# Kernel optimization log

Measured on AMD Instinct MI355X. Metric: run time of the kernel, lower is better.

Reference implementation:

```python
import jax, jax.numpy as jnp
import numpy as np

MASK_FILL = -1e9  # masked_fill_value (avoids NaNs vs -inf)

def setup_inputs() -> dict:
    key = jax.random.key(0)
    k1, k2, k3 = jax.random.split(key, 3)
    B, L, H, E = 4, 2048, 16, 128
    S, D = L, E
    queries = jax.random.normal(k1, (B, L, H, E), dtype=jnp.float32)
    keys = jax.random.normal(k2, (B, S, H, E), dtype=jnp.float32)
    values = jax.random.normal(k3, (B, S, H, D), dtype=jnp.float32)
    return {"queries": queries, "keys": keys, "values": values}

def reference(queries, keys, values):
    B, L, H, E = queries.shape
    S = keys.shape[1]
    scale = 1.0 / jnp.sqrt(jnp.asarray(E, queries.dtype))
    # compute_scores: dot-product scores (B,H,L,S)
    scores = jnp.einsum('blhe,bshe->bhls', queries, keys)
    # causal mask (mask_flag=True, attn_mask=None -> TriangularCausalMask)
    causal = jnp.triu(jnp.ones((L, S), dtype=bool), k=1)  # True above diagonal = masked
    scores = jnp.where(causal[None, None, :, :], MASK_FILL, scores)
    # scale * scores -> softmax (dropout p=0, eval)
    A = jax.nn.softmax(scale * scores, axis=-1)
    # combine_values: (B,H,L,S) x (B,S,H,D) -> (B,L,H,D)
    V = jnp.einsum('bhls,bshd->blhd', A, values)
    return V
```

## Files before the change

### kernel.cpp

```cpp
#include <hip/hip_runtime.h>
#include <hip/hip_bf16.h>

typedef __attribute__((ext_vector_type(4))) float f32x4;
typedef __attribute__((ext_vector_type(2))) float f32x2v;
typedef __attribute__((ext_vector_type(16))) float f32x16;
typedef __attribute__((ext_vector_type(8))) short s16x8;
typedef __attribute__((ext_vector_type(4))) short s16x4;
typedef __attribute__((ext_vector_type(4))) unsigned u32x4v;
typedef __attribute__((ext_vector_type(2))) int i32x2;

static constexpr int Bb = 4, Ll = 2048, Hh = 16, Ee = 128;
static constexpr int RS = Hh * Ee;
static constexpr float SCALE = 0.088388347648318447f;
static constexpr float LOG2E = 1.4426950408889634f;
static constexpr float SCL = SCALE * LOG2E;
static constexpr float MOFF = 26.0f;

static constexpr int KROW = 272;
static constexpr int KBYTES = 32 * KROW;
static constexpr int VROW = 80;
static constexpr int VBYTES = 128 * VROW;
static constexpr int BUFSZ = KBYTES + VBYTES;

__device__ __forceinline__ unsigned pk2bf(float lo, float hi) {
  float2 t = make_float2(lo, hi);
  __hip_bfloat162 b2 = __float22bfloat162_rn(t);
  union { __hip_bfloat162 b; unsigned u; } cv; cv.b = b2;
  return cv.u;
}

__device__ __forceinline__ s16x8 pack8(float a0, float a1, float a2, float a3,
                                       float a4, float a5, float a6, float a7) {
  u32x4v u = { pk2bf(a0,a1), pk2bf(a2,a3), pk2bf(a4,a5), pk2bf(a6,a7) };
  return *(s16x8*)&u;
}

__device__ __forceinline__ void plswap(int &x, int &y, int h5) {
#if __has_builtin(__builtin_amdgcn_permlane32_swap)
  i32x2 r = __builtin_amdgcn_permlane32_swap(x, y, false, false);
  x = r[0]; y = r[1];
#else
  int px = __shfl_xor(x, 32, 64);
  int py = __shfl_xor(y, 32, 64);
  int nx = h5 ? py : x;
  int ny = h5 ? y : px;
  x = nx; y = ny;
#endif
}

__device__ __forceinline__ s16x8 mkpa(float p0, float p1, float p2, float p3,
                                      float p4, float p5, float p6, float p7, int h5) {
  int uA = (int)pk2bf(p0, p1), uB = (int)pk2bf(p2, p3);
  int uC = (int)pk2bf(p4, p5), uD = (int)pk2bf(p6, p7);
  plswap(uA, uC, h5);
  plswap(uB, uD, h5);
  u32x4v u = { (unsigned)uA, (unsigned)uB, (unsigned)uC, (unsigned)uD };
  return *(s16x8*)&u;
}

__device__ __forceinline__ void gl_lds16(const short* g, short* l) {
  __builtin_amdgcn_global_load_lds((const __attribute__((address_space(1))) void*)g,
                                   (__attribute__((address_space(3))) void*)l, 16, 0, 0);
}

__global__ __launch_bounds__(256) void conv_k(const float* __restrict__ src, short* __restrict__ dst) {
  size_t i = ((size_t)blockIdx.x * 256 + threadIdx.x) * 8;
  f32x4 a = *(const f32x4*)(src + i);
  f32x4 b = *(const f32x4*)(src + i + 4);
  *(s16x8*)(dst + i) = pack8(a[0],a[1],a[2],a[3],b[0],b[1],b[2],b[3]);
}

__global__ __launch_bounds__(256) void conv_vt(const float* __restrict__ V, unsigned* __restrict__ Vt32) {
  const int bh = blockIdx.x >> 4, s0 = (blockIdx.x & 15) * 128;
  const int b = bh >> 4, h = bh & 15;
  const int w = threadIdx.x >> 6, lane = threadIdx.x & 63;
  const float* base = V + ((size_t)(b * Ll + s0 + 32 * w)) * RS + h * Ee + 2 * lane;
  unsigned w0[16], w1[16];
#pragma unroll
  for (int j = 0; j < 16; ++j) {
    f32x2v a = *(const f32x2v*)(base + (size_t)(2 * j) * RS);
    f32x2v c = *(const f32x2v*)(base + (size_t)(2 * j + 1) * RS);
    w0[j] = pk2bf(a[0], c[0]);
    w1[j] = pk2bf(a[1], c[1]);
  }
  unsigned* r0 = Vt32 + ((size_t)(bh * 128 + 2 * lane)) * 1024 + (s0 + 32 * w) / 2;
  unsigned* r1 = r0 + 1024;
#pragma unroll
  for (int jj = 0; jj < 4; ++jj) {
    *(u32x4v*)(r0 + 4 * jj) = (u32x4v){w0[4*jj], w0[4*jj+1], w0[4*jj+2], w0[4*jj+3]};
    *(u32x4v*)(r1 + 4 * jj) = (u32x4v){w1[4*jj], w1[4*jj+1], w1[4*jj+2], w1[4*jj+3]};
  }
}

__global__ __launch_bounds__(256, 3)
void attn_main(const float* __restrict__ Qg, const short* __restrict__ Kws,
               const short* __restrict__ Vtws, float* __restrict__ Og) {
  const int phys = blockIdx.x;
  const int qi = ((phys >> 6) & 1) ? (phys >> 7) : (15 - (phys >> 7));
  const int bh = phys & 63;
  const int b = bh >> 4, h = bh & 15;
  const int qb = qi * 128;
  const int tid = threadIdx.x, w = tid >> 6, l = tid & 63;
  const int l31 = l & 31, h5 = l >> 5;

  __shared__ __align__(16) short smem[BUFSZ];

  s16x8 qfrag[8];
  {
    const float* qp = Qg + ((size_t)(b * Ll + qb + 32 * w + l31)) * RS + h * Ee;
#pragma unroll
    for (int ks = 0; ks < 8; ++ks) {
      const int e0 = 16 * ks + 8 * h5;
      f32x4 f0 = *(const f32x4*)(qp + e0);
      f32x4 f1 = *(const f32x4*)(qp + e0 + 4);
      qfrag[ks] = pack8(f0[0]*SCL, f0[1]*SCL, f0[2]*SCL, f0[3]*SCL,
                        f1[0]*SCL, f1[1]*SCL, f1[2]*SCL, f1[3]*SCL);
    }
  }

  f32x16 acc[4];
#pragma unroll
  for (int dt = 0; dt < 4; ++dt)
#pragma unroll
    for (int r = 0; r < 16; ++r) acc[dt][r] = 0.f;
  float lacc = 0.f;

  const short* skp[3]; const short* svp[3];
  int kdst[3], vdst[3];
#pragma unroll
  for (int j = 0; j < 3; ++j) {
    const int kid = (j < 2) ? (w * 136 + 64 * j + l) : (w * 136 + 128 + (l & 7));
    const int kr = kid / 17;
    int ksl = kid % 17; if (ksl == 16) ksl = 0;
    skp[j] = Kws + ((size_t)(b * Ll + kr)) * 2048 + h * 128 + ksl * 8;
    kdst[j] = kid * 16;
    const int vid = (j < 2) ? (w * 160 + 64 * j + l) : (w * 160 + 128 + (l & 31));
    const int vr = vid / 5;
    int vsl = vid % 5; if (vsl == 4) vsl = 0;
    svp[j] = Vtws + ((size_t)(bh * 128 + vr)) * 2048 + vsl * 8;
    vdst[j] = KBYTES + vid * 16;
  }

#define STAGE(cb, kvb) do { \
    gl_lds16(skp[0] + (size_t)(kvb) * 2048, (short*)((char*)smem + (cb) + kdst[0])); \
    gl_lds16(skp[1] + (size_t)(kvb) * 2048, (short*)((char*)smem + (cb) + kdst[1])); \
    if (l < 8)  gl_lds16(skp[2] + (size_t)(kvb) * 2048, (short*)((char*)smem + (cb) + kdst[2])); \
    gl_lds16(svp[0] + (kvb), (short*)((char*)smem + (cb) + vdst[0])); \
    gl_lds16(svp[1] + (kvb), (short*)((char*)smem + (cb) + vdst[1])); \
    if (l < 32) gl_lds16(svp[2] + (kvb), (short*)((char*)smem + (cb) + vdst[2])); \
  } while (0)

  const int ntiles = 4 * qi + 4;
  const int tmaxw = 4 * qi + w;

  STAGE(0, 0);

  for (int t = 0; t < ntiles; ++t) {
    const int cbase = (t & 1) ? BUFSZ : 0;
    if (t + 1 < ntiles) {
      STAGE(cbase ? 0 : BUFSZ, 32 * (t + 1));
      asm volatile("s_waitcnt vmcnt(6)" ::: "memory");
    } else {
      asm volatile("s_waitcnt vmcnt(0)" ::: "memory");
    }
    __builtin_amdgcn_s_barrier();
    __builtin_amdgcn_sched_barrier(0);

    if (t <= tmaxw) {
      f32x16 s;
#pragma unroll
      for (int r = 0; r < 16; ++r) s[r] = 0.f;
      __builtin_amdgcn_s_setprio(1);
#pragma unroll
      for (int ks = 0; ks < 8; ++ks) {
        s16x8 a = *(const s16x8*)((const char*)smem + cbase + l31 * KROW + h5 * 16 + ks * 32);
        s = __builtin_amdgcn_mfma_f32_32x32x16_bf16(a, qfrag[ks], s, 0, 0, 0);
      }
      __builtin_amdgcn_s_setprio(0);

      if (t == tmaxw) {
#pragma unroll
        for (int r = 0; r < 16; ++r) {
          const int kvl = (r & 3) + 8 * (r >> 2) + 4 * h5;
          if (kvl > l31) s[r] = -3.0e38f;
        }
      }

      float pv[16];
#pragma unroll
      for (int r = 0; r < 16; ++r) { const float p2 = exp2f(s[r] - MOFF); pv[r] = p2; lacc += p2; }
      s16x8 pa0 = mkpa(pv[0], pv[1], pv[2], pv[3], pv[4], pv[5], pv[6], pv[7], h5);
      s16x8 pa1 = mkpa(pv[8], pv[9], pv[10], pv[11], pv[12], pv[13], pv[14], pv[15], h5);

      __builtin_amdgcn_s_setprio(1);
#pragma unroll
      for (int dt = 0; dt < 4; ++dt) {
        const int vb = cbase + KBYTES + dt * (32 * VROW) + l31 * VROW + h5 * 16;
        s16x8 av0 = *(const s16x8*)((const char*)smem + vb);
        acc[dt] = __builtin_amdgcn_mfma_f32_32x32x16_bf16(av0, pa0, acc[dt], 0, 0, 0);
        s16x8 av1 = *(const s16x8*)((const char*)smem + vb + 32);
        acc[dt] = __builtin_amdgcn_mfma_f32_32x32x16_bf16(av1, pa1, acc[dt], 0, 0, 0);
      }
      __builtin_amdgcn_s_setprio(0);
    }
    __builtin_amdgcn_sched_barrier(0);
    __builtin_amdgcn_s_barrier();
  }
#undef STAGE

  float lsum;
  {
    int pb = __builtin_bit_cast(int, lacc), pc = pb;
    plswap(pb, pc, h5);
    lsum = __builtin_bit_cast(float, pb) + __builtin_bit_cast(float, pc);
  }
  const float linv = 1.0f / lsum;

  float* orow = Og + ((size_t)(b * Ll + qb + 32 * w + l31)) * RS + h * Ee;
#pragma unroll
  for (int dt = 0; dt < 4; ++dt)
#pragma unroll
    for (int g = 0; g < 4; ++g) {
      f32x4 v = { acc[dt][4*g] * linv, acc[dt][4*g+1] * linv,
                  acc[dt][4*g+2] * linv, acc[dt][4*g+3] * linv };
      *(f32x4*)(orow + dt * 32 + g * 8 + h5 * 4) = v;
    }
}

static constexpr int VPAD = 66;
__device__ __forceinline__ short f2bf(float f) {
  union { float f; unsigned u; } x; x.f = f;
  unsigned r = x.u + 0x7FFFu + ((x.u >> 16) & 1u);
  return (short)(r >> 16);
}
__global__ __launch_bounds__(256, 4)
void attn_fwd(const float* __restrict__ Qg, const float* __restrict__ Kg,
              const float* __restrict__ Vg, float* __restrict__ Og) {
  const int qi = blockIdx.x;
  const int bh = blockIdx.y;
  const int b = bh >> 4, h = bh & 15;
  const int qb = qi * 64;
  const int tid = threadIdx.x, wave = tid >> 6, lane = tid & 63, lo = lane & 15, hi = lane >> 4;
  __shared__ __align__(16) short Klds[64 * 128];
  __shared__ __align__(16) short Vt[128 * VPAD];
  const float* Qb_ = Qg + (size_t)b * Ll * RS + h * Ee;
  const float* Kb_ = Kg + (size_t)b * Ll * RS + h * Ee;
  const float* Vb_ = Vg + (size_t)b * Ll * RS + h * Ee;
  float* Ob_ = Og + (size_t)b * Ll * RS + h * Ee;
  s16x8 qfrag[4];
  {
    const float* qp = Qb_ + (size_t)(qb + wave * 16 + lo) * RS;
#pragma unroll
    for (int ks = 0; ks < 4; ++ks) {
      const int e0 = 32 * ks + 8 * hi;
      f32x4 f0 = *(const f32x4*)(qp + e0);
      f32x4 f1 = *(const f32x4*)(qp + e0 + 4);
      qfrag[ks] = pack8(f0[0]*SCALE, f0[1]*SCALE, f0[2]*SCALE, f0[3]*SCALE,
                        f1[0]*SCALE, f1[1]*SCALE, f1[2]*SCALE, f1[3]*SCALE);
    }
  }
  f32x4 acc[8];
#pragma unroll
  for (int nt = 0; nt < 8; ++nt) acc[nt] = (f32x4){0.f, 0.f, 0.f, 0.f};
  float mrun = -3.0e38f, lrun = 0.f;
  const int r0 = tid >> 4, c0 = (tid & 15) * 8;
  for (int kvb = 0; kvb <= qb; kvb += 64) {
    __syncthreads();
#pragma unroll
    for (int rr4 = 0; rr4 < 4; ++rr4) {
      const int rr = r0 + 16 * rr4;
      const float* kp = Kb_ + (size_t)(kvb + rr) * RS + c0;
      f32x4 f0 = *(const f32x4*)kp;
      f32x4 f1 = *(const f32x4*)(kp + 4);
      const int off = (rr * 256 + c0 * 2) ^ ((rr & 7) << 4);
      *(s16x8*)((char*)Klds + off) = pack8(f0[0],f0[1],f0[2],f0[3],f1[0],f1[1],f1[2],f1[3]);
    }
#pragma unroll
    for (int kk = 0; kk < 2; ++kk) {
      const int kv0 = (r0 * 2 + kk) * 2;
      const float* vp0 = Vb_ + (size_t)(kvb + kv0) * RS + c0;
      const float* vp1 = vp0 + RS;
      f32x4 a0 = *(const f32x4*)vp0, a1 = *(const f32x4*)(vp0 + 4);
      f32x4 b0 = *(const f32x4*)vp1, b1 = *(const f32x4*)(vp1 + 4);
#pragma unroll
      for (int j = 0; j < 4; ++j)
        *(unsigned*)&Vt[(c0 + j) * VPAD + kv0] = pk2bf(a0[j], b0[j]);
#pragma unroll
      for (int j = 0; j < 4; ++j)
        *(unsigned*)&Vt[(c0 + 4 + j) * VPAD + kv0] = pk2bf(a1[j], b1[j]);
    }
    __syncthreads();
    const bool diag = (kvb == qb);
    f32x4 st[4];
#pragma unroll
    for (int mt = 0; mt < 4; ++mt) {
      f32x4 a4 = (f32x4){0.f, 0.f, 0.f, 0.f};
#pragma unroll
      for (int ks = 0; ks < 4; ++ks) {
        const int row = 16 * mt + lo;
        const int off = (row * 256 + (32 * ks + 8 * hi) * 2) ^ ((row & 7) << 4);
        s16x8 a = *(const s16x8*)((const char*)Klds + off);
        a4 = __builtin_amdgcn_mfma_f32_16x16x32_bf16(a, qfrag[ks], a4, 0, 0, 0);
      }
      st[mt] = a4;
    }
    if (diag) {
      const int qg = 16 * wave + lo;
#pragma unroll
      for (int mt = 0; mt < 4; ++mt)
#pragma unroll
        for (int r = 0; r < 4; ++r)
          if (16 * mt + 4 * hi + r > qg) st[mt][r] = -3.0e38f;
    }
    float mx = -3.0e38f;
#pragma unroll
    for (int mt = 0; mt < 4; ++mt)
#pragma unroll
      for (int r = 0; r < 4; ++r) mx = fmaxf(mx, st[mt][r]);
    mx = fmaxf(mx, __shfl_xor(mx, 16, 64));
    mx = fmaxf(mx, __shfl_xor(mx, 32, 64));
    const float mnew = fmaxf(mrun, mx);
    const float alpha = exp2f((mrun - mnew) * LOG2E);
    float psum = 0.f;
    s16x4 pf[4];
#pragma unroll
    for (int mt = 0; mt < 4; ++mt)
#pragma unroll
      for (int r = 0; r < 4; ++r) {
        const float p = exp2f((st[mt][r] - mnew) * LOG2E);
        psum += p;
        pf[mt][r] = f2bf(p);
      }
    psum += __shfl_xor(psum, 16, 64);
    psum += __shfl_xor(psum, 32, 64);
    lrun = lrun * alpha + psum;
    mrun = mnew;
    float alr[4];
#pragma unroll
    for (int r = 0; r < 4; ++r) alr[r] = __shfl(alpha, 4 * hi + r, 64);
#pragma unroll
    for (int nt = 0; nt < 8; ++nt) {
      acc[nt][0] *= alr[0]; acc[nt][1] *= alr[1];
      acc[nt][2] *= alr[2]; acc[nt][3] *= alr[3];
    }
#pragma unroll
    for (int mt = 0; mt < 4; ++mt)
#pragma unroll
      for (int nt = 0; nt < 8; ++nt) {
        const int hw = (16 * nt + lo) * VPAD + 16 * mt + 4 * hi;
        s16x4 vf = *(const s16x4*)&Vt[hw];
        acc[nt] = __builtin_amdgcn_mfma_f32_16x16x16bf16_1k(pf[mt], vf, acc[nt], 0, 0, 0);
      }
  }
  float linv[4];
#pragma unroll
  for (int r = 0; r < 4; ++r) linv[r] = 1.0f / __shfl(lrun, 4 * hi + r, 64);
#pragma unroll
  for (int r = 0; r < 4; ++r) {
    const int qg = qb + 16 * wave + 4 * hi + r;
    float* op = Ob_ + (size_t)qg * RS + lo;
#pragma unroll
    for (int nt = 0; nt < 8; ++nt)
      op[16 * nt] = acc[nt][r] * linv[r];
  }
}

extern "C" void kernel_launch(void* const* d_in, const int* in_sizes, int n_in,
                              void* d_out, int out_size, void* d_ws, size_t ws_size,
                              hipStream_t stream) {
  const float* Qp = (const float*)d_in[0];
  const float* Kp = (const float*)d_in[1];
  const float* Vp = (const float*)d_in[2];
  float* Op = (float*)d_out;
  const size_t elems = (size_t)Bb * Ll * Hh * Ee;
  if (ws_size >= elems * 2 * 2) {
    short* Kws = (short*)d_ws;
    short* Vtws = Kws + elems;
    conv_k<<<(int)(elems / 8 / 256), 256, 0, stream>>>(Kp, Kws);
    conv_vt<<<Bb * Hh * (Ll / 128), 256, 0, stream>>>(Vp, (unsigned*)Vtws);
    attn_main<<<1024, 256, 0, stream>>>(Qp, Kws, Vtws, Op);
  } else {
    dim3 grid(Ll / 64, Bb * Hh);
    attn_fwd<<<grid, 256, 0, stream>>>(Qp, Kp, Vp, Op);
  }
}
```

Before: 157.9 us.

## Use 512-thread blocks over 256-row query tiles with paired causal work

The attention kernel now uses 8 waves per block, so each block covers 256 query rows and shares each staged K/V tile across twice as many waves. Each block processes two query tiles (j and 7-j) in sequence, which evens out causal work across a grid of 256 blocks, replacing the earlier interleaved 1024-block ordering. Staging per thread is reduced to match the larger block. The grid drops to 256 blocks, which may underfill the GPU's compute units and lengthen the serial per-block tail. Per-tile synchronisation now spans 8 waves, some of which sit idle on diagonal tiles.

Result: slower. 166.2 us (+5.3%).

```diff
diff --git a/kernel.cpp b/kernel.cpp
--- a/kernel.cpp
+++ b/kernel.cpp
@@ -92,139 +92,147 @@
   }
 }
 
-__global__ __launch_bounds__(256, 3)
+__global__ __launch_bounds__(512, 2)
 void attn_main(const float* __restrict__ Qg, const short* __restrict__ Kws,
                const short* __restrict__ Vtws, float* __restrict__ Og) {
   const int phys = blockIdx.x;
-  const int qi = ((phys >> 6) & 1) ? (phys >> 7) : (15 - (phys >> 7));
   const int bh = phys & 63;
+  const int j = phys >> 6;
   const int b = bh >> 4, h = bh & 15;
-  const int qb = qi * 128;
   const int tid = threadIdx.x, w = tid >> 6, l = tid & 63;
   const int l31 = l & 31, h5 = l >> 5;
 
   __shared__ __align__(16) short smem[BUFSZ];
 
-  s16x8 qfrag[8];
+  const short* skp[2]; const short* svp[2];
+  int kdst[2], vdst[2];
   {
-    const float* qp = Qg + ((size_t)(b * Ll + qb + 32 * w + l31)) * RS + h * Ee;
-#pragma unroll
-    for (int ks = 0; ks < 8; ++ks) {
-      const int e0 = 16 * ks + 8 * h5;
-      f32x4 f0 = *(const f32x4*)(qp + e0);
-      f32x4 f1 = *(const f32x4*)(qp + e0 + 4);
-      qfrag[ks] = pack8(f0[0]*SCL, f0[1]*SCL, f0[2]*SCL, f0[3]*SCL,
-                        f1[0]*SCL, f1[1]*SCL, f1[2]*SCL, f1[3]*SCL);
-    }
-  }
-
-  f32x16 acc[4];
-#pragma unroll
-  for (int dt = 0; dt < 4; ++dt)
-#pragma unroll
-    for (int r = 0; r < 16; ++r) acc[dt][r] = 0.f;
-  float lacc = 0.f;
-
-  const short* skp[3]; const short* svp[3];
-  int kdst[3], vdst[3];
-#pragma unroll
-  for (int j = 0; j < 3; ++j) {
-    const int kid = (j < 2) ? (w * 136 + 64 * j + l) : (w * 136 + 128 + (l & 7));
-    const int kr = kid / 17;
-    int ksl = kid % 17; if (ksl == 16) ksl = 0;
-    skp[j] = Kws + ((size_t)(b * Ll + kr)) * 2048 + h * 128 + ksl * 8;
-    kdst[j] = kid * 16;
-    const int vid = (j < 2) ? (w * 160 + 64 * j + l) : (w * 160 + 128 + (l & 31));
-    const int vr = vid / 5;
-    int vsl = vid % 5; if (vsl == 4) vsl = 0;
-    svp[j] = Vtws + ((size_t)(bh * 128 + vr)) * 2048 + vsl * 8;
-    vdst[j] = KBYTES + vid * 16;
+    const int kid0 = w * 68 + l;
+    const int kid1 = w * 68 + 64 + (l & 3);
+    const int vid0 = w * 80 + l;
+    const int vid1 = w * 80 + 64 + (l & 15);
+    const int kids[2] = { kid0, kid1 };
+    const int vids[2] = { vid0, vid1 };
+#pragma unroll
+    for (int i = 0; i < 2; ++i) {
+      const int kr = kids[i] / 17;
+      int ksl = kids[i] % 17; if (ksl == 16) ksl = 0;
+      skp[i] = Kws + ((size_t)(b * Ll + kr)) * 2048 + h * 128 + ksl * 8;
+      kdst[i] = kids[i] * 16;
+      const int vr = vids[i] / 5;
+      int vsl = vids[i] % 5; if (vsl == 4) vsl = 0;
+      svp[i] = Vtws + ((size_t)(bh * 128 + vr)) * 2048 + vsl * 8;
+      vdst[i] = KBYTES + vids[i] * 16;
+    }
   }
 
 #define STAGE(cb, kvb) do { \
     gl_lds16(skp[0] + (size_t)(kvb) * 2048, (short*)((char*)smem + (cb) + kdst[0])); \
-    gl_lds16(skp[1] + (size_t)(kvb) * 2048, (short*)((char*)smem + (cb) + kdst[1])); \
-    if (l < 8)  gl_lds16(skp[2] + (size_t)(kvb) * 2048, (short*)((char*)smem + (cb) + kdst[2])); \
+    if (l < 4)  gl_lds16(skp[1] + (size_t)(kvb) * 2048, (short*)((char*)smem + (cb) + kdst[1])); \
     gl_lds16(svp[0] + (kvb), (short*)((char*)smem + (cb) + vdst[0])); \
-    gl_lds16(svp[1] + (kvb), (short*)((char*)smem + (cb) + vdst[1])); \
-    if (l < 32) gl_lds16(svp[2] + (kvb), (short*)((char*)smem + (cb) + vdst[2])); \
+    if (l < 16) gl_lds16(svp[1] + (kvb), (short*)((char*)smem + (cb) + vdst[1])); \
   } while (0)
 
-  const int ntiles = 4 * qi + 4;
-  const int tmaxw = 4 * qi + w;
-
-  STAGE(0, 0);
-
-  for (int t = 0; t < ntiles; ++t) {
-    const int cbase = (t & 1) ? BUFSZ : 0;
-    if (t + 1 < ntiles) {
-      STAGE(cbase ? 0 : BUFSZ, 32 * (t + 1));
-      asm volatile("s_waitcnt vmcnt(6)" ::: "memory");
-    } else {
-      asm volatile("s_waitcnt vmcnt(0)" ::: "memory");
-    }
-    __builtin_amdgcn_s_barrier();
-    __builtin_amdgcn_sched_barrier(0);
-
-    if (t <= tmaxw) {
-      f32x16 s;
-#pragma unroll
-      for (int r = 0; r < 16; ++r) s[r] = 0.f;
-      __builtin_amdgcn_s_setprio(1);
+  for (int p = 0; p < 2; ++p) {
+    const int qi = p ? (7 - j) : j;
+    const int qb = qi * 256;
+
+    s16x8 qfrag[8];
+    {
+      const float* qp = Qg + ((size_t)(b * Ll + qb + 32 * w + l31)) * RS + h * Ee;
 #pragma unroll
       for (int ks = 0; ks < 8; ++ks) {
-        s16x8 a = *(const s16x8*)((const char*)smem + cbase + l31 * KROW + h5 * 16 + ks * 32);
-        s = __builtin_amdgcn_mfma_f32_32x32x16_bf16(a, qfrag[ks], s, 0, 0, 0);
-      }
-      __builtin_amdgcn_s_setprio(0);
-
-      if (t == tmaxw) {
-#pragma unroll
-        for (int r = 0; r < 16; ++r) {
-          const int kvl = (r & 3) + 8 * (r >> 2) + 4 * h5;
-          if (kvl > l31) s[r] = -3.0e38f;
+        const int e0 = 16 * ks + 8 * h5;
+        f32x4 f0 = *(const f32x4*)(qp + e0);
+        f32x4 f1 = *(const f32x4*)(qp + e0 + 4);
+        qfrag[ks] = pack8(f0[0]*SCL, f0[1]*SCL, f0[2]*SCL, f0[3]*SCL,
+                          f1[0]*SCL, f1[1]*SCL, f1[2]*SCL, f1[3]*SCL);
+      }
+    }
+
+    f32x16 acc[4];
+#pragma unroll
+    for (int dt = 0; dt < 4; ++dt)
+#pragma unroll
+      for (int r = 0; r < 16; ++r) acc[dt][r] = 0.f;
+    float lacc = 0.f;
+
+    const int ntiles = 8 * qi + 8;
+    const int tmaxw = 8 * qi + w;
+
+    STAGE(0, 0);
+
+    for (int t = 0; t < ntiles; ++t) {
+      const int cbase = (t & 1) ? BUFSZ : 0;
+      if (t + 1 < ntiles) {
+        STAGE(cbase ? 0 : BUFSZ, 32 * (t + 1));
+        asm volatile("s_waitcnt vmcnt(4)" ::: "memory");
+      } else {
+        asm volatile("s_waitcnt vmcnt(0)" ::: "memory");
+      }
+      __builtin_amdgcn_s_barrier();
+      __builtin_amdgcn_sched_barrier(0);
+
+      if (t <= tmaxw) {
+        f32x16 s;
+#pragma unroll
+        for (int r = 0; r < 16; ++r) s[r] = 0.f;
+        __builtin_amdgcn_s_setprio(1);
+#pragma unroll
+        for (int ks = 0; ks < 8; ++ks) {
+          s16x8 a = *(const s16x8*)((const char*)smem + cbase + l31 * KROW + h5 * 16 + ks * 32);
+          s = __builtin_amdgcn_mfma_f32_32x32x16_bf16(a, qfrag[ks], s, 0, 0, 0);
         }
-      }
-
-      float pv[16];
-#pragma unroll
-      for (int r = 0; r < 16; ++r) { const float p2 = exp2f(s[r] - MOFF); pv[r] = p2; lacc += p2; }
-      s16x8 pa0 = mkpa(pv[0], pv[1], pv[2], pv[3], pv[4], pv[5], pv[6], pv[7], h5);
-      s16x8 pa1 = mkpa(pv[8], pv[9], pv[10], pv[11], pv[12], pv[13], pv[14], pv[15], h5);
-
-      __builtin_amdgcn_s_setprio(1);
-#pragma unroll
-      for (int dt = 0; dt < 4; ++dt) {
-        const int vb = cbase + KBYTES + dt * (32 * VROW) + l31 * VROW + h5 * 16;
-        s16x8 av0 = *(const s16x8*)((const char*)smem + vb);
-        acc[dt] = __builtin_amdgcn_mfma_f32_32x32x16_bf16(av0, pa0, acc[dt], 0, 0, 0);
-        s16x8 av1 = *(const s16x8*)((const char*)smem + vb + 32);
-        acc[dt] = __builtin_amdgcn_mfma_f32_32x32x16_bf16(av1, pa1, acc[dt], 0, 0, 0);
-      }
-      __builtin_amdgcn_s_setprio(0);
-    }
-    __builtin_amdgcn_sched_barrier(0);
-    __builtin_amdgcn_s_barrier();
+        __builtin_amdgcn_s_setprio(0);
+
+        if (t == tmaxw) {
+#pragma unroll
+          for (int r = 0; r < 16; ++r) {
+            const int kvl = (r & 3) + 8 * (r >> 2) + 4 * h5;
+            if (kvl > l31) s[r] = -3.0e38f;
+          }
+        }
+
+        float pv[16];
+#pragma unroll
+        for (int r = 0; r < 16; ++r) { const float p2 = exp2f(s[r] - MOFF); pv[r] = p2; lacc += p2; }
+        s16x8 pa0 = mkpa(pv[0], pv[1], pv[2], pv[3], pv[4], pv[5], pv[6], pv[7], h5);
+        s16x8 pa1 = mkpa(pv[8], pv[9], pv[10], pv[11], pv[12], pv[13], pv[14], pv[15], h5);
+
+        __builtin_amdgcn_s_setprio(1);
+#pragma unroll
+        for (int dt = 0; dt < 4; ++dt) {
+          const int vb = cbase + KBYTES + dt * (32 * VROW) + l31 * VROW + h5 * 16;
+          s16x8 av0 = *(const s16x8*)((const char*)smem + vb);
+          acc[dt] = __builtin_amdgcn_mfma_f32_32x32x16_bf16(av0, pa0, acc[dt], 0, 0, 0);
+          s16x8 av1 = *(const s16x8*)((const char*)smem + vb + 32);
+          acc[dt] = __builtin_amdgcn_mfma_f32_32x32x16_bf16(av1, pa1, acc[dt], 0, 0, 0);
+        }
+        __builtin_amdgcn_s_setprio(0);
+      }
+      __builtin_amdgcn_sched_barrier(0);
+      __builtin_amdgcn_s_barrier();
+    }
+
+    float lsum;
+    {
+      int pb = __builtin_bit_cast(int, lacc), pc = pb;
+      plswap(pb, pc, h5);
+      lsum = __builtin_bit_cast(float, pb) + __builtin_bit_cast(float, pc);
+    }
+    const float linv = 1.0f / lsum;
+
+    float* orow = Og + ((size_t)(b * Ll + qb + 32 * w + l31)) * RS + h * Ee;
+#pragma unroll
+    for (int dt = 0; dt < 4; ++dt)
+#pragma unroll
+      for (int g = 0; g < 4; ++g) {
+        f32x4 v = { acc[dt][4*g] * linv, acc[dt][4*g+1] * linv,
+                    acc[dt][4*g+2] * linv, acc[dt][4*g+3] * linv };
+        *(f32x4*)(orow + dt * 32 + g * 8 + h5 * 4) = v;
+      }
   }
 #undef STAGE
-
-  float lsum;
-  {
-    int pb = __builtin_bit_cast(int, lacc), pc = pb;
-    plswap(pb, pc, h5);
-    lsum = __builtin_bit_cast(float, pb) + __builtin_bit_cast(float, pc);
-  }
-  const float linv = 1.0f / lsum;
-
-  float* orow = Og + ((size_t)(b * Ll + qb + 32 * w + l31)) * RS + h * Ee;
-#pragma unroll
-  for (int dt = 0; dt < 4; ++dt)
-#pragma unroll
-    for (int g = 0; g < 4; ++g) {
-      f32x4 v = { acc[dt][4*g] * linv, acc[dt][4*g+1] * linv,
-                  acc[dt][4*g+2] * linv, acc[dt][4*g+3] * linv };
-      *(f32x4*)(orow + dt * 32 + g * 8 + h5 * 4) = v;
-    }
 }
 
 static constexpr int VPAD = 66;
@@ -283,11 +291,11 @@
       f32x4 a0 = *(const f32x4*)vp0, a1 = *(const f32x4*)(vp0 + 4);
       f32x4 b0 = *(const f32x4*)vp1, b1 = *(const f32x4*)(vp1 + 4);
 #pragma unroll
-      for (int j = 0; j < 4; ++j)
-        *(unsigned*)&Vt[(c0 + j) * VPAD + kv0] = pk2bf(a0[j], b0[j]);
-#pragma unroll
-      for (int j = 0; j < 4; ++j)
-        *(unsigned*)&Vt[(c0 + 4 + j) * VPAD + kv0] = pk2bf(a1[j], b1[j]);
+      for (int jj = 0; jj < 4; ++jj)
+        *(unsigned*)&Vt[(c0 + jj) * VPAD + kv0] = pk2bf(a0[jj], b0[jj]);
+#pragma unroll
+      for (int jj = 0; jj < 4; ++jj)
+        *(unsigned*)&Vt[(c0 + 4 + jj) * VPAD + kv0] = pk2bf(a1[jj], b1[jj]);
     }
     __syncthreads();
     const bool diag = (kvb == qb);
@@ -378,7 +386,7 @@
     short* Vtws = Kws + elems;
     conv_k<<<(int)(elems / 8 / 256), 256, 0, stream>>>(Kp, Kws);
     conv_vt<<<Bb * Hh * (Ll / 128), 256, 0, stream>>>(Vp, (unsigned*)Vtws);
-    attn_main<<<1024, 256, 0, stream>>>(Qp, Kws, Vtws, Op);
+    attn_main<<<256, 512, 0, stream>>>(Qp, Kws, Vtws, Op);
   } else {
     dim3 grid(Ll / 64, Bb * Hh);
     attn_fwd<<<grid, 256, 0, stream>>>(Qp, Kp, Vp, Op);
```
